# Optimization experiments

Measured on AMD Instinct MI355X. Metric: run time of the kernel, lower is better.

## Reference

```python
import jax, jax.numpy as jnp
import numpy as np

B, C, D = 1024, 50000, 256
LR = 0.5


def setup_inputs() -> dict:
    key = jax.random.key(0)
    kx, kl, kc = jax.random.split(key, 3)
    x = jax.random.normal(kx, (B, D), dtype=jnp.float32)
    labels = jax.random.randint(kl, (B,), 0, C)
    y = jax.nn.one_hot(labels, C, dtype=jnp.float32)  # [B, C] one-hot
    center = jax.random.normal(kc, (C, D), dtype=jnp.float32) * 0.05
    return {"x": x, "y": y, "center": center}


def reference(x, y, center):
    # dists = x - y @ center : gather each sample's class center via one-hot GEMM
    dists = x - jnp.matmul(y, center)                      # [B, D]
    # center gradient: scatter-add of -dists into class rows via one-hot GEMM
    grads = jnp.matmul(-y.T, dists)                        # [C, D]
    new_center = center - LR * grads                       # manual SGD update (assign_sub)
    loss = jnp.linalg.norm(dists, axis=1, keepdims=True)   # [B, 1]
    num_sams = jnp.sum(y, axis=0, keepdims=True) + 1.0     # [1, C]
    loss = loss / num_sams                                 # broadcasts to [B, C] as in original
    return loss, new_center
```

## Files before the change

### kernel.cpp

```cpp
#include <hip/hip_runtime.h>
#include <math.h>

#define BB 1024
#define CC 50000
#define DD 256
#define LRATE 0.5f

__global__ void k_init(const float4* __restrict__ center,
                       float4* __restrict__ out_center,
                       int4* __restrict__ counts) {
    int i = blockIdx.x * blockDim.x + threadIdx.x;
    const int n4 = CC * DD / 4;
    if (i < n4) out_center[i] = center[i];
    if (i < CC / 4)
        counts[i] = make_int4(0, 0, 0, 0);
}

#define CHUNK_ITERS 8
__global__ void k_labels_update(const unsigned int* __restrict__ y,
                                const float* __restrict__ x,
                                const float* __restrict__ center,
                                float* __restrict__ out_center,
                                int* __restrict__ counts,
                                float* __restrict__ loss_norm) {
    int b = blockIdx.x;
    const uint4* row = (const uint4*)(y + (size_t)b * CC);
    __shared__ int s_lab;
    __shared__ float s_part[4];
    if (threadIdx.x == 0) s_lab = -1;
    __syncthreads();

    const int C4 = CC / 4;
    for (int base = 0; base < C4; base += 256 * CHUNK_ITERS) {
        #pragma unroll
        for (int j = 0; j < CHUNK_ITERS; ++j) {
            int i = base + j * 256 + threadIdx.x;
            if (i < C4) {
                uint4 v = row[i];
                if (v.x | v.y | v.z | v.w) {
                    s_lab = 4 * i + (v.x ? 0 : (v.y ? 1 : (v.z ? 2 : 3)));
                }
            }
        }
        __syncthreads();
        int found = s_lab;
        __syncthreads();
        if (found >= 0) break;
    }

    int lab = s_lab;
    if (lab < 0) lab = 0;
    if (threadIdx.x == 0) atomicAdd(&counts[lab], 1);

    int d = threadIdx.x;
    float dist = x[(size_t)b * DD + d] - center[(size_t)lab * DD + d];
    atomicAdd(&out_center[(size_t)lab * DD + d], LRATE * dist);

    float sq = dist * dist;
    #pragma unroll
    for (int off = 32; off > 0; off >>= 1)
        sq += __shfl_down(sq, off, 64);
    if ((threadIdx.x & 63) == 0) s_part[threadIdx.x >> 6] = sq;
    __syncthreads();
    if (threadIdx.x == 0)
        loss_norm[b] = sqrtf(s_part[0] + s_part[1] + s_part[2] + s_part[3]);
}

#define ROWS_PER_BLK 16
__global__ void k_loss(const float* __restrict__ loss_norm,
                       const int* __restrict__ counts,
                       float* __restrict__ out_loss) {
    const int C4 = CC / 4;
    int c4 = blockIdx.x * blockDim.x + threadIdx.x;
    if (c4 >= C4) return;
    int4 cnt = ((const int4*)counts)[c4];
    float4 inv;
    inv.x = 1.0f / ((float)cnt.x + 1.0f);
    inv.y = 1.0f / ((float)cnt.y + 1.0f);
    inv.z = 1.0f / ((float)cnt.z + 1.0f);
    inv.w = 1.0f / ((float)cnt.w + 1.0f);
    int b0 = blockIdx.y * ROWS_PER_BLK;
    #pragma unroll
    for (int r = 0; r < ROWS_PER_BLK; ++r) {
        int b = b0 + r;
        float ln = loss_norm[b];
        float4 o;
        o.x = ln * inv.x; o.y = ln * inv.y; o.z = ln * inv.z; o.w = ln * inv.w;
        ((float4*)(out_loss + (size_t)b * CC))[c4] = o;
    }
}

extern "C" void kernel_launch(void* const* d_in, const int* in_sizes, int n_in,
                              void* d_out, int out_size, void* d_ws, size_t ws_size,
                              hipStream_t stream) {
    const float* x      = (const float*)d_in[0];
    const unsigned int* y = (const unsigned int*)d_in[1];
    const float* center = (const float*)d_in[2];

    float* out_loss   = (float*)d_out;
    float* out_center = (float*)d_out + (size_t)BB * CC;

    int*   counts    = (int*)d_ws;
    float* loss_norm = (float*)((char*)d_ws + 256 * 1024);

    k_init<<<CC * DD / 4 / 256, 256, 0, stream>>>(
        (const float4*)center, (float4*)out_center, (int4*)counts);

    k_labels_update<<<BB, DD, 0, stream>>>(
        y, x, center, out_center, counts, loss_norm);

    dim3 lgrid((CC / 4 + 255) / 256, BB / ROWS_PER_BLK);
    k_loss<<<lgrid, 256, 0, stream>>>(loss_norm, counts, out_loss);
}
```

Before: 420.0 us.

## Fuse center copy into label scan and move scatter/histogram into loss kernel

The separate init kernel goes away. The center copy now runs on extra blocks of the label-scan kernel, so it overlaps with the scan of the one-hot matrix. Per-class counts are rebuilt as a shared-memory histogram inside each loss block from a compact label array, which removes the global count atomics and zeroing. The atomic center update is deferred to the loss kernel using stored distances. This saves one launch and the global zeroing pass, but each loss block re-reads all 1024 labels, and the scatter now shares time with the large loss write.

```diff
diff --git a/kernel.cpp b/kernel.cpp
--- a/kernel.cpp
+++ b/kernel.cpp
@@ -6,24 +6,24 @@
 #define DD 256
 #define LRATE 0.5f
 
-__global__ void k_init(const float4* __restrict__ center,
-                       float4* __restrict__ out_center,
-                       int4* __restrict__ counts) {
-    int i = blockIdx.x * blockDim.x + threadIdx.x;
-    const int n4 = CC * DD / 4;
-    if (i < n4) out_center[i] = center[i];
-    if (i < CC / 4)
-        counts[i] = make_int4(0, 0, 0, 0);
-}
-
-#define CHUNK_ITERS 8
-__global__ void k_labels_update(const unsigned int* __restrict__ y,
-                                const float* __restrict__ x,
-                                const float* __restrict__ center,
-                                float* __restrict__ out_center,
-                                int* __restrict__ counts,
-                                float* __restrict__ loss_norm) {
-    int b = blockIdx.x;
+#define CHUNK_ITERS 4
+__global__ void k_scan_copy(const unsigned int* __restrict__ y,
+                            const float* __restrict__ x,
+                            const float* __restrict__ center,
+                            float4* __restrict__ out_center,
+                            int* __restrict__ labels,
+                            float* __restrict__ dist_ws,
+                            float* __restrict__ loss_norm) {
+    int blk = blockIdx.x;
+    if (blk >= BB) {
+        int cb = blk - BB;
+        const float4* src = (const float4*)center;
+        const int n4 = CC * DD / 4;
+        for (int i = cb * 256 + threadIdx.x; i < n4; i += BB * 256)
+            out_center[i] = src[i];
+        return;
+    }
+    int b = blk;
     const uint4* row = (const uint4*)(y + (size_t)b * CC);
     __shared__ int s_lab;
     __shared__ float s_part[4];
@@ -37,9 +37,8 @@
             int i = base + j * 256 + threadIdx.x;
             if (i < C4) {
                 uint4 v = row[i];
-                if (v.x | v.y | v.z | v.w) {
+                if (v.x | v.y | v.z | v.w)
                     s_lab = 4 * i + (v.x ? 0 : (v.y ? 1 : (v.z ? 2 : 3)));
-                }
             }
         }
         __syncthreads();
@@ -50,11 +49,10 @@
 
     int lab = s_lab;
     if (lab < 0) lab = 0;
-    if (threadIdx.x == 0) atomicAdd(&counts[lab], 1);
-
     int d = threadIdx.x;
     float dist = x[(size_t)b * DD + d] - center[(size_t)lab * DD + d];
-    atomicAdd(&out_center[(size_t)lab * DD + d], LRATE * dist);
+    dist_ws[(size_t)b * DD + d] = dist;
+    if (threadIdx.x == 0) labels[b] = lab;
 
     float sq = dist * dist;
     #pragma unroll
@@ -67,48 +65,72 @@
 }
 
 #define ROWS_PER_BLK 16
-__global__ void k_loss(const float* __restrict__ loss_norm,
-                       const int* __restrict__ counts,
-                       float* __restrict__ out_loss) {
+__global__ void k_loss_scatter(const float* __restrict__ loss_norm,
+                               const int* __restrict__ labels,
+                               const float* __restrict__ dist_ws,
+                               float* __restrict__ out_loss,
+                               float* __restrict__ out_center) {
+    __shared__ int histo[1024];
+    const int tid = threadIdx.x;
+    const int c0 = blockIdx.x * 1024;
+    #pragma unroll
+    for (int j = tid; j < 1024; j += 256) histo[j] = 0;
+    __syncthreads();
+    {
+        int4 lb = ((const int4*)labels)[tid];
+        int l;
+        l = lb.x - c0; if ((unsigned)l < 1024u) atomicAdd(&histo[l], 1);
+        l = lb.y - c0; if ((unsigned)l < 1024u) atomicAdd(&histo[l], 1);
+        l = lb.z - c0; if ((unsigned)l < 1024u) atomicAdd(&histo[l], 1);
+        l = lb.w - c0; if ((unsigned)l < 1024u) atomicAdd(&histo[l], 1);
+    }
+    __syncthreads();
+
     const int C4 = CC / 4;
-    int c4 = blockIdx.x * blockDim.x + threadIdx.x;
-    if (c4 >= C4) return;
-    int4 cnt = ((const int4*)counts)[c4];
-    float4 inv;
-    inv.x = 1.0f / ((float)cnt.x + 1.0f);
-    inv.y = 1.0f / ((float)cnt.y + 1.0f);
-    inv.z = 1.0f / ((float)cnt.z + 1.0f);
-    inv.w = 1.0f / ((float)cnt.w + 1.0f);
-    int b0 = blockIdx.y * ROWS_PER_BLK;
-    #pragma unroll
-    for (int r = 0; r < ROWS_PER_BLK; ++r) {
-        int b = b0 + r;
-        float ln = loss_norm[b];
-        float4 o;
-        o.x = ln * inv.x; o.y = ln * inv.y; o.z = ln * inv.z; o.w = ln * inv.w;
-        ((float4*)(out_loss + (size_t)b * CC))[c4] = o;
+    int c4 = blockIdx.x * 256 + tid;
+    if (c4 < C4) {
+        float4 inv;
+        inv.x = 1.0f / ((float)histo[4 * tid + 0] + 1.0f);
+        inv.y = 1.0f / ((float)histo[4 * tid + 1] + 1.0f);
+        inv.z = 1.0f / ((float)histo[4 * tid + 2] + 1.0f);
+        inv.w = 1.0f / ((float)histo[4 * tid + 3] + 1.0f);
+        int b0 = blockIdx.y * ROWS_PER_BLK;
+        #pragma unroll
+        for (int r = 0; r < ROWS_PER_BLK; ++r) {
+            int b = b0 + r;
+            float ln = loss_norm[b];
+            float4 o;
+            o.x = ln * inv.x; o.y = ln * inv.y; o.z = ln * inv.z; o.w = ln * inv.w;
+            ((float4*)(out_loss + (size_t)b * CC))[c4] = o;
+        }
+    }
+
+    int fid = blockIdx.y * gridDim.x + blockIdx.x;
+    if (fid < BB) {
+        int lab = labels[fid];
+        float dv = dist_ws[(size_t)fid * DD + tid];
+        atomicAdd(&out_center[(size_t)lab * DD + tid], LRATE * dv);
     }
 }
 
 extern "C" void kernel_launch(void* const* d_in, const int* in_sizes, int n_in,
                               void* d_out, int out_size, void* d_ws, size_t ws_size,
                               hipStream_t stream) {
-    const float* x      = (const float*)d_in[0];
+    const float* x        = (const float*)d_in[0];
     const unsigned int* y = (const unsigned int*)d_in[1];
-    const float* center = (const float*)d_in[2];
+    const float* center   = (const float*)d_in[2];
 
     float* out_loss   = (float*)d_out;
     float* out_center = (float*)d_out + (size_t)BB * CC;
 
-    int*   counts    = (int*)d_ws;
-    float* loss_norm = (float*)((char*)d_ws + 256 * 1024);
+    int*   labels    = (int*)d_ws;
+    float* dist_ws   = (float*)((char*)d_ws + 4096);
+    float* loss_norm = (float*)((char*)d_ws + 4096 + (size_t)BB * DD * 4);
 
-    k_init<<<CC * DD / 4 / 256, 256, 0, stream>>>(
-        (const float4*)center, (float4*)out_center, (int4*)counts);
-
-    k_labels_update<<<BB, DD, 0, stream>>>(
-        y, x, center, out_center, counts, loss_norm);
+    k_scan_copy<<<2 * BB, DD, 0, stream>>>(
+        y, x, center, (float4*)out_center, labels, dist_ws, loss_norm);
 
     dim3 lgrid((CC / 4 + 255) / 256, BB / ROWS_PER_BLK);
-    k_loss<<<lgrid, 256, 0, stream>>>(loss_norm, counts, out_loss);
+    k_loss_scatter<<<lgrid, 256, 0, stream>>>(
+        loss_norm, labels, dist_ws, out_loss, out_center);
 }
```

New measurement: 421.4 us. About the same (+0.3%).
